# Optimization experiments

Hardware: AMD Instinct MI355X
Metric: run time of the kernel (lower is better)

Reference implementation:

```python
import jax, jax.numpy as jnp
import numpy as np

SPARSITY_RATIO = 0.1


def setup_inputs() -> dict:
    key = jax.random.key(0)
    x = jax.random.normal(key, (4, 4096, 2048), dtype=jnp.float32)
    return {"x": x}


def reference(x):
    # x: [batch, seq_len, n_embd]
    B, S, D = x.shape
    k = max(1, int(D * SPARSITY_RATIO))
    # top-k by absolute value along the feature dim
    _, topk_idx = jax.lax.top_k(jnp.abs(x), k)  # [B, S, k]
    # scatter 1.0 at top-k positions (matches torch scatter_ mask construction)
    b = jnp.arange(B)[:, None, None]
    s = jnp.arange(S)[None, :, None]
    mask = jnp.zeros_like(x).at[b, s, topk_idx].set(1.0)
    scale = jnp.asarray(D / k, dtype=x.dtype)
    return x * mask * scale
```

## Files before the change

### kernel.cpp

```cpp
#include <hip/hip_runtime.h>


constexpr int D_DIM = 2048;
constexpr int K_SEL = 204;
constexpr int NT    = 256;
constexpr int EPL   = 32;

__device__ __forceinline__ int dpp_reduce_add(int x) {
    x += __builtin_amdgcn_update_dpp(0, x, 0x111, 0xF, 0xF, true);
    x += __builtin_amdgcn_update_dpp(0, x, 0x112, 0xF, 0xF, true);
    x += __builtin_amdgcn_update_dpp(0, x, 0x114, 0xF, 0xF, true);
    x += __builtin_amdgcn_update_dpp(0, x, 0x118, 0xF, 0xF, true);
    x += __builtin_amdgcn_update_dpp(0, x, 0x142, 0xA, 0xF, false);
    x += __builtin_amdgcn_update_dpp(0, x, 0x143, 0xC, 0xF, false);
    return __builtin_amdgcn_readlane(x, 63);
}

__global__ __launch_bounds__(NT) void sparse_topk_kernel(const float* __restrict__ x,
                                                         float* __restrict__ out) {
    const int wave = threadIdx.x >> 6;
    const int lane = threadIdx.x & 63;
    const long long row = (long long)blockIdx.x * 4 + wave;
    const float* xr = x + row * D_DIM;
    float* outr = out + row * D_DIM;

    unsigned a[EPL];
    unsigned signs = 0u;
    const float4* xp = reinterpret_cast<const float4*>(xr);
#pragma unroll
    for (int b = 0; b < 8; ++b) {
        const float4 f = xp[b * 64 + lane];
        const unsigned w0 = __float_as_uint(f.x), w1 = __float_as_uint(f.y);
        const unsigned w2 = __float_as_uint(f.z), w3 = __float_as_uint(f.w);
        a[4 * b + 0] = w0 & 0x7fffffffu; signs |= (w0 >> 31) << (4 * b + 0);
        a[4 * b + 1] = w1 & 0x7fffffffu; signs |= (w1 >> 31) << (4 * b + 1);
        a[4 * b + 2] = w2 & 0x7fffffffu; signs |= (w2 >> 31) << (4 * b + 2);
        a[4 * b + 3] = w3 & 0x7fffffffu; signs |= (w3 >> 31) << (4 * b + 3);
    }

    const float scale = 2048.0f / 204.0f;

    unsigned T = 0u;
    unsigned thr = 0u;
    bool done = false;
#pragma unroll 1
    for (int bit = 30; bit >= 0; --bit) {
        const unsigned test = T | (1u << bit);
        int c0 = 0, c1 = 0, c2 = 0, c3 = 0;
#pragma unroll
        for (int j = 0; j < EPL; j += 4) {
            c0 += (a[j + 0] >= test) ? 1 : 0;
            c1 += (a[j + 1] >= test) ? 1 : 0;
            c2 += (a[j + 2] >= test) ? 1 : 0;
            c3 += (a[j + 3] >= test) ? 1 : 0;
        }
        const int cnt = dpp_reduce_add((c0 + c1) + (c2 + c3));
        if (cnt == K_SEL) { thr = test; done = true; break; }
        if (cnt > K_SEL) T = test;
    }

    float v[EPL];

    if (done) {
#pragma unroll
        for (int j = 0; j < EPL; ++j) {
            const float val =
                __uint_as_float(a[j] | (((signs >> j) & 1u) << 31)) * scale;
            v[j] = (a[j] >= thr) ? val : 0.0f;
        }
    } else {
        int ge_pack = 0;
#pragma unroll
        for (int j = 0; j < EPL; ++j) {
            ge_pack += (a[j] > T) ? 1 : 0;
            ge_pack += (a[j] == T) ? (1 << 16) : 0;
        }
        const int tot = dpp_reduce_add(ge_pack);
        const int cnt_gt = tot & 0xFFFF;
        const int neq = tot >> 16;
        const int r = K_SEL - cnt_gt;

        if (neq == r) {
#pragma unroll
            for (int j = 0; j < EPL; ++j) {
                const float val =
                    __uint_as_float(a[j] | (((signs >> j) & 1u) << 31)) * scale;
                v[j] = (a[j] >= T) ? val : 0.0f;
            }
        } else {
            const unsigned long long lt =
                (lane == 0) ? 0ull : (~0ull >> (64 - lane));
            int base = 0;
            for (int b = 0; b < 8; ++b) {
                unsigned long long m[4];
#pragma unroll
                for (int e = 0; e < 4; ++e) m[e] = __ballot(a[4 * b + e] == T);
                int cm = 0;
#pragma unroll
                for (int e = 0; e < 4; ++e) cm += __popcll(m[e] & lt);
                int partial = 0;
#pragma unroll
                for (int e = 0; e < 4; ++e) {
                    const int j = 4 * b + e;
                    const int rank = base + cm + partial;
                    const bool eq = (a[j] == T);
                    const bool sel = (a[j] > T) || (eq && rank < r);
                    const float val =
                        __uint_as_float(a[j] | (((signs >> j) & 1u) << 31)) * scale;
                    v[j] = sel ? val : 0.0f;
                    partial += (int)((m[e] >> lane) & 1ull);
                }
#pragma unroll
                for (int e = 0; e < 4; ++e) base += __popcll(m[e]);
            }
        }
    }

    float4* op = reinterpret_cast<float4*>(outr);
#pragma unroll
    for (int b = 0; b < 8; ++b)
        op[b * 64 + lane] = make_float4(v[4 * b + 0], v[4 * b + 1],
                                        v[4 * b + 2], v[4 * b + 3]);
}

extern "C" void kernel_launch(void* const* d_in, const int* in_sizes, int n_in,
                              void* d_out, int out_size, void* d_ws, size_t ws_size,
                              hipStream_t stream) {
    const float* x = (const float*)d_in[0];
    float* out = (float*)d_out;
    const int rows = in_sizes[0] / D_DIM;
    sparse_topk_kernel<<<rows / 4, NT, 0, stream>>>(x, out);
}
```

Baseline: 235.5 us.

## Process two rows per wave with interleaved radix-select threshold search

Each wave now loads two rows and runs their bitwise threshold searches in the same loop, so the two independent DPP reductions and compare chains can overlap and hide each other's latency. The grid is halved to match. Output stores are now issued per float4 chunk inside a shared finish routine instead of after buffering the whole row. The cost is roughly double the register use per thread, which lowers occupancy, and a row that resolves early keeps iterating until the slower row of its pair finishes.

```diff
diff --git a/kernel.cpp b/kernel.cpp
--- a/kernel.cpp
+++ b/kernel.cpp
@@ -16,59 +16,13 @@
     return __builtin_amdgcn_readlane(x, 63);
 }
 
-__global__ __launch_bounds__(NT) void sparse_topk_kernel(const float* __restrict__ x,
-                                                         float* __restrict__ out) {
-    const int wave = threadIdx.x >> 6;
-    const int lane = threadIdx.x & 63;
-    const long long row = (long long)blockIdx.x * 4 + wave;
-    const float* xr = x + row * D_DIM;
-    float* outr = out + row * D_DIM;
+__device__ __forceinline__ void finish_row(const unsigned (&a)[EPL], unsigned signs,
+                                           bool done, unsigned thr, unsigned T,
+                                           float* __restrict__ outr, int lane) {
+    const float scale = 2048.0f / 204.0f;
+    float4* op = reinterpret_cast<float4*>(outr);
 
-    unsigned a[EPL];
-    unsigned signs = 0u;
-    const float4* xp = reinterpret_cast<const float4*>(xr);
-#pragma unroll
-    for (int b = 0; b < 8; ++b) {
-        const float4 f = xp[b * 64 + lane];
-        const unsigned w0 = __float_as_uint(f.x), w1 = __float_as_uint(f.y);
-        const unsigned w2 = __float_as_uint(f.z), w3 = __float_as_uint(f.w);
-        a[4 * b + 0] = w0 & 0x7fffffffu; signs |= (w0 >> 31) << (4 * b + 0);
-        a[4 * b + 1] = w1 & 0x7fffffffu; signs |= (w1 >> 31) << (4 * b + 1);
-        a[4 * b + 2] = w2 & 0x7fffffffu; signs |= (w2 >> 31) << (4 * b + 2);
-        a[4 * b + 3] = w3 & 0x7fffffffu; signs |= (w3 >> 31) << (4 * b + 3);
-    }
-
-    const float scale = 2048.0f / 204.0f;
-
-    unsigned T = 0u;
-    unsigned thr = 0u;
-    bool done = false;
-#pragma unroll 1
-    for (int bit = 30; bit >= 0; --bit) {
-        const unsigned test = T | (1u << bit);
-        int c0 = 0, c1 = 0, c2 = 0, c3 = 0;
-#pragma unroll
-        for (int j = 0; j < EPL; j += 4) {
-            c0 += (a[j + 0] >= test) ? 1 : 0;
-            c1 += (a[j + 1] >= test) ? 1 : 0;
-            c2 += (a[j + 2] >= test) ? 1 : 0;
-            c3 += (a[j + 3] >= test) ? 1 : 0;
-        }
-        const int cnt = dpp_reduce_add((c0 + c1) + (c2 + c3));
-        if (cnt == K_SEL) { thr = test; done = true; break; }
-        if (cnt > K_SEL) T = test;
-    }
-
-    float v[EPL];
-
-    if (done) {
-#pragma unroll
-        for (int j = 0; j < EPL; ++j) {
-            const float val =
-                __uint_as_float(a[j] | (((signs >> j) & 1u) << 31)) * scale;
-            v[j] = (a[j] >= thr) ? val : 0.0f;
-        }
-    } else {
+    if (!done) {
         int ge_pack = 0;
 #pragma unroll
         for (int j = 0; j < EPL; ++j) {
@@ -80,14 +34,7 @@
         const int neq = tot >> 16;
         const int r = K_SEL - cnt_gt;
 
-        if (neq == r) {
-#pragma unroll
-            for (int j = 0; j < EPL; ++j) {
-                const float val =
-                    __uint_as_float(a[j] | (((signs >> j) & 1u) << 31)) * scale;
-                v[j] = (a[j] >= T) ? val : 0.0f;
-            }
-        } else {
+        if (neq != r) {
             const unsigned long long lt =
                 (lane == 0) ? 0ull : (~0ull >> (64 - lane));
             int base = 0;
@@ -99,6 +46,7 @@
 #pragma unroll
                 for (int e = 0; e < 4; ++e) cm += __popcll(m[e] & lt);
                 int partial = 0;
+                float v[4];
 #pragma unroll
                 for (int e = 0; e < 4; ++e) {
                     const int j = 4 * b + e;
@@ -107,20 +55,99 @@
                     const bool sel = (a[j] > T) || (eq && rank < r);
                     const float val =
                         __uint_as_float(a[j] | (((signs >> j) & 1u) << 31)) * scale;
-                    v[j] = sel ? val : 0.0f;
+                    v[e] = sel ? val : 0.0f;
                     partial += (int)((m[e] >> lane) & 1ull);
                 }
+                op[b * 64 + lane] = make_float4(v[0], v[1], v[2], v[3]);
 #pragma unroll
                 for (int e = 0; e < 4; ++e) base += __popcll(m[e]);
             }
+            return;
         }
+        thr = T;
     }
 
-    float4* op = reinterpret_cast<float4*>(outr);
 #pragma unroll
-    for (int b = 0; b < 8; ++b)
-        op[b * 64 + lane] = make_float4(v[4 * b + 0], v[4 * b + 1],
-                                        v[4 * b + 2], v[4 * b + 3]);
+    for (int b = 0; b < 8; ++b) {
+        float v[4];
+#pragma unroll
+        for (int e = 0; e < 4; ++e) {
+            const int j = 4 * b + e;
+            const float val =
+                __uint_as_float(a[j] | (((signs >> j) & 1u) << 31)) * scale;
+            v[e] = (a[j] >= thr) ? val : 0.0f;
+        }
+        op[b * 64 + lane] = make_float4(v[0], v[1], v[2], v[3]);
+    }
+}
+
+__global__ __launch_bounds__(NT) void sparse_topk_kernel(const float* __restrict__ x,
+                                                         float* __restrict__ out) {
+    const int wave = threadIdx.x >> 6;
+    const int lane = threadIdx.x & 63;
+    const long long rowA = (long long)blockIdx.x * 8 + wave * 2;
+    const float* xA = x + rowA * D_DIM;
+    float* oA = out + rowA * D_DIM;
+
+    unsigned A[EPL], B[EPL];
+    unsigned sA = 0u, sB = 0u;
+    const float4* pA = reinterpret_cast<const float4*>(xA);
+    const float4* pB = reinterpret_cast<const float4*>(xA + D_DIM);
+#pragma unroll
+    for (int b = 0; b < 8; ++b) {
+        const float4 f = pA[b * 64 + lane];
+        const unsigned w0 = __float_as_uint(f.x), w1 = __float_as_uint(f.y);
+        const unsigned w2 = __float_as_uint(f.z), w3 = __float_as_uint(f.w);
+        A[4 * b + 0] = w0 & 0x7fffffffu; sA |= (w0 >> 31) << (4 * b + 0);
+        A[4 * b + 1] = w1 & 0x7fffffffu; sA |= (w1 >> 31) << (4 * b + 1);
+        A[4 * b + 2] = w2 & 0x7fffffffu; sA |= (w2 >> 31) << (4 * b + 2);
+        A[4 * b + 3] = w3 & 0x7fffffffu; sA |= (w3 >> 31) << (4 * b + 3);
+    }
+#pragma unroll
+    for (int b = 0; b < 8; ++b) {
+        const float4 f = pB[b * 64 + lane];
+        const unsigned w0 = __float_as_uint(f.x), w1 = __float_as_uint(f.y);
+        const unsigned w2 = __float_as_uint(f.z), w3 = __float_as_uint(f.w);
+        B[4 * b + 0] = w0 & 0x7fffffffu; sB |= (w0 >> 31) << (4 * b + 0);
+        B[4 * b + 1] = w1 & 0x7fffffffu; sB |= (w1 >> 31) << (4 * b + 1);
+        B[4 * b + 2] = w2 & 0x7fffffffu; sB |= (w2 >> 31) << (4 * b + 2);
+        B[4 * b + 3] = w3 & 0x7fffffffu; sB |= (w3 >> 31) << (4 * b + 3);
+    }
+
+    unsigned TA = 0u, TB = 0u, thrA = 0u, thrB = 0u;
+    bool doneA = false, doneB = false;
+#pragma unroll 1
+    for (int bit = 30; bit >= 0; --bit) {
+        const unsigned tA = TA | (1u << bit);
+        const unsigned tB = TB | (1u << bit);
+        int c0 = 0, c1 = 0, c2 = 0, c3 = 0;
+        int d0 = 0, d1 = 0, d2 = 0, d3 = 0;
+#pragma unroll
+        for (int j = 0; j < EPL; j += 4) {
+            c0 += (A[j + 0] >= tA) ? 1 : 0;
+            c1 += (A[j + 1] >= tA) ? 1 : 0;
+            c2 += (A[j + 2] >= tA) ? 1 : 0;
+            c3 += (A[j + 3] >= tA) ? 1 : 0;
+            d0 += (B[j + 0] >= tB) ? 1 : 0;
+            d1 += (B[j + 1] >= tB) ? 1 : 0;
+            d2 += (B[j + 2] >= tB) ? 1 : 0;
+            d3 += (B[j + 3] >= tB) ? 1 : 0;
+        }
+        const int cntA = dpp_reduce_add((c0 + c1) + (c2 + c3));
+        const int cntB = dpp_reduce_add((d0 + d1) + (d2 + d3));
+        if (!doneA) {
+            if (cntA == K_SEL)     { thrA = tA; doneA = true; }
+            else if (cntA > K_SEL) { TA = tA; }
+        }
+        if (!doneB) {
+            if (cntB == K_SEL)     { thrB = tB; doneB = true; }
+            else if (cntB > K_SEL) { TB = tB; }
+        }
+        if (doneA && doneB) break;
+    }
+
+    finish_row(A, sA, doneA, thrA, TA, oA, lane);
+    finish_row(B, sB, doneB, thrB, TB, oA + D_DIM, lane);
 }
 
 extern "C" void kernel_launch(void* const* d_in, const int* in_sizes, int n_in,
@@ -129,5 +156,5 @@
     const float* x = (const float*)d_in[0];
     float* out = (float*)d_out;
     const int rows = in_sizes[0] / D_DIM;
-    sparse_topk_kernel<<<rows / 4, NT, 0, stream>>>(x, out);
+    sparse_topk_kernel<<<rows / 8, NT, 0, stream>>>(x, out);
 }
```

After: 244.9 us. +4.0%, slower.

## Process four rows per wave with next-row prefetch and seeded threshold search

Applied to the files above, without the earlier changes.

Each wave now handles four consecutive rows. It loads the next row's data into registers while running the threshold search on the current row, so global-load latency is hidden behind compute. The radix-style bit search is replaced by a bisection over the float bit range, seeded with guesses near the expected 90th-percentile magnitude of a standard normal, so an exact count of 204 may be found in fewer steps. Output is written per float4 chunk rather than buffered in a full register array. The grid is four times smaller, which lowers the number of resident waves available for latency hiding.

```diff
diff --git a/kernel.cpp b/kernel.cpp
--- a/kernel.cpp
+++ b/kernel.cpp
@@ -5,6 +5,7 @@
 constexpr int K_SEL = 204;
 constexpr int NT    = 256;
 constexpr int EPL   = 32;
+constexpr int RPW   = 4;
 
 __device__ __forceinline__ int dpp_reduce_add(int x) {
     x += __builtin_amdgcn_update_dpp(0, x, 0x111, 0xF, 0xF, true);
@@ -16,59 +17,25 @@
     return __builtin_amdgcn_readlane(x, 63);
 }
 
-__global__ __launch_bounds__(NT) void sparse_topk_kernel(const float* __restrict__ x,
-                                                         float* __restrict__ out) {
-    const int wave = threadIdx.x >> 6;
-    const int lane = threadIdx.x & 63;
-    const long long row = (long long)blockIdx.x * 4 + wave;
-    const float* xr = x + row * D_DIM;
-    float* outr = out + row * D_DIM;
+__device__ __forceinline__ int count_ge(const unsigned (&a)[EPL], unsigned t) {
+    int c0 = 0, c1 = 0, c2 = 0, c3 = 0;
+#pragma unroll
+    for (int j = 0; j < EPL; j += 4) {
+        c0 += (a[j + 0] >= t) ? 1 : 0;
+        c1 += (a[j + 1] >= t) ? 1 : 0;
+        c2 += (a[j + 2] >= t) ? 1 : 0;
+        c3 += (a[j + 3] >= t) ? 1 : 0;
+    }
+    return dpp_reduce_add((c0 + c1) + (c2 + c3));
+}
 
-    unsigned a[EPL];
-    unsigned signs = 0u;
-    const float4* xp = reinterpret_cast<const float4*>(xr);
-#pragma unroll
-    for (int b = 0; b < 8; ++b) {
-        const float4 f = xp[b * 64 + lane];
-        const unsigned w0 = __float_as_uint(f.x), w1 = __float_as_uint(f.y);
-        const unsigned w2 = __float_as_uint(f.z), w3 = __float_as_uint(f.w);
-        a[4 * b + 0] = w0 & 0x7fffffffu; signs |= (w0 >> 31) << (4 * b + 0);
-        a[4 * b + 1] = w1 & 0x7fffffffu; signs |= (w1 >> 31) << (4 * b + 1);
-        a[4 * b + 2] = w2 & 0x7fffffffu; signs |= (w2 >> 31) << (4 * b + 2);
-        a[4 * b + 3] = w3 & 0x7fffffffu; signs |= (w3 >> 31) << (4 * b + 3);
-    }
+__device__ __forceinline__ void finish_row(const unsigned (&a)[EPL], unsigned signs,
+                                           bool exact, unsigned thr, unsigned T,
+                                           float* __restrict__ outr, int lane) {
+    const float scale = 2048.0f / 204.0f;
+    float4* op = reinterpret_cast<float4*>(outr);
 
-    const float scale = 2048.0f / 204.0f;
-
-    unsigned T = 0u;
-    unsigned thr = 0u;
-    bool done = false;
-#pragma unroll 1
-    for (int bit = 30; bit >= 0; --bit) {
-        const unsigned test = T | (1u << bit);
-        int c0 = 0, c1 = 0, c2 = 0, c3 = 0;
-#pragma unroll
-        for (int j = 0; j < EPL; j += 4) {
-            c0 += (a[j + 0] >= test) ? 1 : 0;
-            c1 += (a[j + 1] >= test) ? 1 : 0;
-            c2 += (a[j + 2] >= test) ? 1 : 0;
-            c3 += (a[j + 3] >= test) ? 1 : 0;
-        }
-        const int cnt = dpp_reduce_add((c0 + c1) + (c2 + c3));
-        if (cnt == K_SEL) { thr = test; done = true; break; }
-        if (cnt > K_SEL) T = test;
-    }
-
-    float v[EPL];
-
-    if (done) {
-#pragma unroll
-        for (int j = 0; j < EPL; ++j) {
-            const float val =
-                __uint_as_float(a[j] | (((signs >> j) & 1u) << 31)) * scale;
-            v[j] = (a[j] >= thr) ? val : 0.0f;
-        }
-    } else {
+    if (!exact) {
         int ge_pack = 0;
 #pragma unroll
         for (int j = 0; j < EPL; ++j) {
@@ -80,14 +47,7 @@
         const int neq = tot >> 16;
         const int r = K_SEL - cnt_gt;
 
-        if (neq == r) {
-#pragma unroll
-            for (int j = 0; j < EPL; ++j) {
-                const float val =
-                    __uint_as_float(a[j] | (((signs >> j) & 1u) << 31)) * scale;
-                v[j] = (a[j] >= T) ? val : 0.0f;
-            }
-        } else {
+        if (neq != r) {
             const unsigned long long lt =
                 (lane == 0) ? 0ull : (~0ull >> (64 - lane));
             int base = 0;
@@ -99,6 +59,7 @@
 #pragma unroll
                 for (int e = 0; e < 4; ++e) cm += __popcll(m[e] & lt);
                 int partial = 0;
+                float v[4];
 #pragma unroll
                 for (int e = 0; e < 4; ++e) {
                     const int j = 4 * b + e;
@@ -107,20 +68,90 @@
                     const bool sel = (a[j] > T) || (eq && rank < r);
                     const float val =
                         __uint_as_float(a[j] | (((signs >> j) & 1u) << 31)) * scale;
-                    v[j] = sel ? val : 0.0f;
+                    v[e] = sel ? val : 0.0f;
                     partial += (int)((m[e] >> lane) & 1ull);
                 }
+                op[b * 64 + lane] = make_float4(v[0], v[1], v[2], v[3]);
 #pragma unroll
                 for (int e = 0; e < 4; ++e) base += __popcll(m[e]);
             }
+            return;
         }
+        thr = T;
     }
 
-    float4* op = reinterpret_cast<float4*>(outr);
 #pragma unroll
-    for (int b = 0; b < 8; ++b)
-        op[b * 64 + lane] = make_float4(v[4 * b + 0], v[4 * b + 1],
-                                        v[4 * b + 2], v[4 * b + 3]);
+    for (int b = 0; b < 8; ++b) {
+        float v[4];
+#pragma unroll
+        for (int e = 0; e < 4; ++e) {
+            const int j = 4 * b + e;
+            const float val =
+                __uint_as_float(a[j] | (((signs >> j) & 1u) << 31)) * scale;
+            v[e] = (a[j] >= thr) ? val : 0.0f;
+        }
+        op[b * 64 + lane] = make_float4(v[0], v[1], v[2], v[3]);
+    }
+}
+
+__global__ __launch_bounds__(NT) void sparse_topk_kernel(const float* __restrict__ x,
+                                                         float* __restrict__ out) {
+    const int wave = threadIdx.x >> 6;
+    const int lane = threadIdx.x & 63;
+    const long long wid = (long long)blockIdx.x * 4 + wave;
+    const float* base = x + wid * RPW * D_DIM;
+    float* obase = out + wid * RPW * D_DIM;
+
+    float4 nf[8];
+    {
+        const float4* p = reinterpret_cast<const float4*>(base);
+#pragma unroll
+        for (int b = 0; b < 8; ++b) nf[b] = p[b * 64 + lane];
+    }
+
+#pragma unroll 1
+    for (int r = 0; r < RPW; ++r) {
+        unsigned a[EPL];
+        unsigned signs = 0u;
+#pragma unroll
+        for (int b = 0; b < 8; ++b) {
+            const unsigned w0 = __float_as_uint(nf[b].x);
+            const unsigned w1 = __float_as_uint(nf[b].y);
+            const unsigned w2 = __float_as_uint(nf[b].z);
+            const unsigned w3 = __float_as_uint(nf[b].w);
+            a[4 * b + 0] = w0 & 0x7fffffffu; signs |= (w0 >> 31) << (4 * b + 0);
+            a[4 * b + 1] = w1 & 0x7fffffffu; signs |= (w1 >> 31) << (4 * b + 1);
+            a[4 * b + 2] = w2 & 0x7fffffffu; signs |= (w2 >> 31) << (4 * b + 2);
+            a[4 * b + 3] = w3 & 0x7fffffffu; signs |= (w3 >> 31) << (4 * b + 3);
+        }
+
+        if (r + 1 < RPW) {
+            const float4* pn = reinterpret_cast<const float4*>(base + (r + 1) * D_DIM);
+#pragma unroll
+            for (int b = 0; b < 8; ++b) nf[b] = pn[b * 64 + lane];
+        }
+
+        unsigned lo = 0u, hi = 0x7F800000u;
+        unsigned thr = 0u;
+        bool exact = false;
+        int step = 0, lastcnt = 0;
+#pragma unroll 1
+        while (hi - lo > 1u) {
+            unsigned mid;
+            if (step == 0)      mid = 0x3FD28F5Cu;
+            else if (step == 1) mid = (lastcnt > K_SEL) ? 0x3FE66666u
+                                                        : 0x3FC00000u;
+            else                mid = lo + ((hi - lo) >> 1);
+            if (mid <= lo || mid >= hi) mid = lo + ((hi - lo) >> 1);
+            ++step;
+            const int cnt = count_ge(a, mid);
+            lastcnt = cnt;
+            if (cnt == K_SEL) { thr = mid; exact = true; break; }
+            if (cnt > K_SEL) lo = mid; else hi = mid;
+        }
+
+        finish_row(a, signs, exact, thr, lo, obase + (long long)r * D_DIM, lane);
+    }
 }
 
 extern "C" void kernel_launch(void* const* d_in, const int* in_sizes, int n_in,
@@ -129,5 +160,6 @@
     const float* x = (const float*)d_in[0];
     float* out = (float*)d_out;
     const int rows = in_sizes[0] / D_DIM;
-    sparse_topk_kernel<<<rows / 4, NT, 0, stream>>>(x, out);
+    const int blocks = rows / (RPW * 4);
+    sparse_topk_kernel<<<blocks, NT, 0, stream>>>(x, out);
 }
```

Result: slower. 242.9 us (+3.1%).
